# Kernel tuning notes

Measured on AMD Instinct MI355X. Metric: run time of the kernel, lower is better.

Reference implementation:

```python
import jax, jax.numpy as jnp
import numpy as np

C = 512
CQK = C // 8  # 64


def setup_inputs() -> dict:
    key = jax.random.key(0)
    ks = jax.random.split(key, 7)
    s = 0.02
    x = jax.random.normal(ks[0], (4, C, 64, 64), dtype=jnp.float32)
    Wq = jax.random.normal(ks[1], (CQK, C), dtype=jnp.float32) * s
    bq = jnp.zeros((CQK,), dtype=jnp.float32)
    Wk = jax.random.normal(ks[2], (CQK, C), dtype=jnp.float32) * s
    bk = jnp.zeros((CQK,), dtype=jnp.float32)
    Wv = jax.random.normal(ks[3], (C, C), dtype=jnp.float32) * s
    bv = jnp.zeros((C,), dtype=jnp.float32)
    return {"x": x, "Wq": Wq, "bq": bq, "Wk": Wk, "bk": bk, "Wv": Wv, "bv": bv}


def reference(x, Wq, bq, Wk, bk, Wv, bv):
    B, Cc, W, H = x.shape
    N = W * H
    xf = x.reshape(B, Cc, N)  # [B, C, N]
    # 1x1 convs are channel-wise matmuls
    q = jnp.einsum('oc,bcn->bon', Wq, xf) + bq[None, :, None]  # [B, CQK, N]
    k = jnp.einsum('oc,bcn->bon', Wk, xf) + bk[None, :, None]  # [B, CQK, N]
    v = jnp.einsum('oc,bcn->bon', Wv, xf) + bv[None, :, None]  # [B, C, N]
    # attention[b, i, j] = softmax_j(q_i . k_j)
    scores = jnp.einsum('bqi,bqj->bij', q, k)  # [B, N, N]
    attn = jax.nn.softmax(scores, axis=-1)
    # out[b, c, i] = sum_j v[b, c, j] * attn[b, i, j]
    out = jnp.einsum('bcj,bij->bci', v, attn)
    return out.reshape(B, Cc, W, H) + x
```

## Files before the change

kernel.cpp:

```cpp
#include <hip/hip_runtime.h>


typedef __attribute__((ext_vector_type(8))) short bf16x8;
typedef __attribute__((ext_vector_type(4))) float f32x4;

#define MFMA16(A, B, C) __builtin_amdgcn_mfma_f32_16x16x32_bf16((A), (B), (C), 0, 0, 0)
#define MFMA8(A, B, C) __builtin_amdgcn_mfma_f32_16x16x32_fp8_fp8((long)(A), (long)(B), (C), 0, 0, 0)

__device__ __forceinline__ ushort f2bf(float f) {
  uint u = __builtin_bit_cast(uint, f);
  u = (u + 0x7FFFu + ((u >> 16) & 1u)) >> 16;
  return (ushort)u;
}

__device__ __forceinline__ void gload_lds16(const void* g, void* l) {
  __builtin_amdgcn_global_load_lds(
      (const __attribute__((address_space(1))) void*)g,
      (__attribute__((address_space(3))) void*)l, 16, 0, 0);
}

__device__ __forceinline__ void lds_barrier() {
  __builtin_amdgcn_sched_barrier(0);
  asm volatile("s_waitcnt lgkmcnt(0)" ::: "memory");
  __builtin_amdgcn_s_barrier();
  __builtin_amdgcn_sched_barrier(0);
}

__global__ void wconv(const float* __restrict__ Wq, const float* __restrict__ Wk,
                      const float* __restrict__ Wv, ushort* __restrict__ Wb) {
  const int row = blockIdx.x;
  const int t = threadIdx.x;
  const float* src = row < 64 ? Wq + (size_t)row * 512
                   : row < 128 ? Wk + (size_t)(row - 64) * 512
                               : Wv + (size_t)(row - 128) * 512;
  const float4 f = *reinterpret_cast<const float4*>(src + t * 4);
  ushort4 u;
  u.x = f2bf(f.x); u.y = f2bf(f.y); u.z = f2bf(f.z); u.w = f2bf(f.w);
  *reinterpret_cast<ushort4*>(Wb + (size_t)row * 512 + t * 4) = u;
}

__global__ __launch_bounds__(512, 1) void qkv_fused(
    const float* __restrict__ x, const ushort* __restrict__ Wb,
    const float* __restrict__ bq, const float* __restrict__ bk,
    const float* __restrict__ bv,
    ushort* __restrict__ q, ushort* __restrict__ k, uchar* __restrict__ v) {
  __shared__ ushort xT[64][72];

  const int bid = blockIdx.x;
  const int xcd = bid & 7;
  const int b = xcd >> 1;
  const int n0 = ((bid >> 3) + ((xcd & 1) << 5)) * 64;
  const int tid = threadIdx.x;
  const int w = tid >> 6, l = tid & 63;
  const int l15 = l & 15, l16 = l >> 4;

  const float* xb = x + (size_t)b * 512 * 4096 + n0;

  float xr[8];
#define LOADX(CH0)                                              \
  _Pragma("unroll") for (int p = 0; p < 8; ++p)                 \
      xr[p] = xb[((size_t)((CH0) + w * 8 + p)) * 4096 + l];

  LOADX(0);

  const f32x4 fz = {0.f, 0.f, 0.f, 0.f};
  f32x4 acc[4][5];
#pragma unroll
  for (int a = 0; a < 4; ++a)
#pragma unroll
    for (int o = 0; o < 5; ++o) acc[a][o] = fz;

  for (int ck = 0; ck < 8; ++ck) {
    bf16x8 xw;
#pragma unroll
    for (int p = 0; p < 8; ++p) xw[p] = (short)f2bf(xr[p]);
    *reinterpret_cast<bf16x8*>(&xT[l][w * 8]) = xw;
    lds_barrier();
    if (ck < 7) {
      const int c1 = (ck + 1) * 64;
      LOADX(c1);
    }
#pragma unroll
    for (int kk = 0; kk < 2; ++kk) {
      bf16x8 a[4];
#pragma unroll
      for (int nf = 0; nf < 4; ++nf)
        a[nf] = *reinterpret_cast<const bf16x8*>(&xT[nf * 16 + l15][kk * 32 + l16 * 8]);
#pragma unroll
      for (int oi = 0; oi < 5; ++oi) {
        const bf16x8 bw = *reinterpret_cast<const bf16x8*>(
            &Wb[(size_t)(w * 80 + oi * 16 + l15) * 512 + ck * 64 + kk * 32 + l16 * 8]);
#pragma unroll
        for (int nf = 0; nf < 4; ++nf) acc[nf][oi] = MFMA16(a[nf], bw, acc[nf][oi]);
      }
    }
    lds_barrier();
  }

#pragma unroll
  for (int oi = 0; oi < 5; ++oi) {
    const int obase = w * 80 + oi * 16;
    const int orow = obase + l15;
    if (obase < 64) {
      const float bias = bq[orow];
      ushort* dq = q + ((size_t)b * 4096 + n0) * 64;
#pragma unroll
      for (int nf = 0; nf < 4; ++nf)
#pragma unroll
        for (int r = 0; r < 4; ++r)
          dq[(size_t)(nf * 16 + l16 * 4 + r) * 64 + orow] = f2bf(acc[nf][oi][r] + bias);
    } else if (obase < 128) {
      const float bias = bk[orow - 64];
      ushort* dk = k + ((size_t)b * 4096 + n0) * 64;
#pragma unroll
      for (int nf = 0; nf < 4; ++nf)
#pragma unroll
        for (int r = 0; r < 4; ++r)
          dk[(size_t)(nf * 16 + l16 * 4 + r) * 64 + (orow - 64)] = f2bf(acc[nf][oi][r] + bias);
    } else {
      const int c = orow - 128;
      const float bias = bv[c];
#pragma unroll
      for (int nf = 0; nf < 4; ++nf) {
        uint u = 0;
        u = __builtin_amdgcn_cvt_pk_fp8_f32(acc[nf][oi][0] + bias, acc[nf][oi][1] + bias, u, false);
        u = __builtin_amdgcn_cvt_pk_fp8_f32(acc[nf][oi][2] + bias, acc[nf][oi][3] + bias, u, true);
        *reinterpret_cast<uint*>(&v[((size_t)b * 512 + c) * 4096 + n0 + nf * 16 + l16 * 4]) = u;
      }
    }
  }
}

__global__ __launch_bounds__(256, 2) void attn_kernel(
    const float* __restrict__ x, const ushort* __restrict__ q,
    const ushort* __restrict__ k, const uchar* __restrict__ v,
    float* __restrict__ out) {
  __shared__ uchar vbuf[2][32768];
  __shared__ uchar kbuf[2][8192];

  const int bid = blockIdx.x;
  const int xcd = bid & 7;
  const int b = xcd >> 1;
  const int i0 = ((bid >> 3) + ((xcd & 1) << 6)) * 32;
  const int tid = threadIdx.x;
  const int w = tid >> 6, l = tid & 63;
  const int l15 = l & 15, l16 = l >> 4;
  const int hi = l >> 5;
  const int rg = w & 1, ch = w >> 1;
  const int i0w = i0 + rg * 16;
  const int c0 = ch * 256;

  const uchar* kbb = (const uchar*)(k + (size_t)b * 4096 * 64);
  const uchar* vg = v + (size_t)b * 512 * 4096;

  bf16x8 qf0, qf1;
  {
    const ushort* qp = q + ((size_t)b * 4096 + i0w + l15) * 64 + l16 * 8;
    qf0 = *reinterpret_cast<const bf16x8*>(qp);
    qf1 = *reinterpret_cast<const bf16x8*>(qp + 32);
  }

  const int vrow = tid >> 2;
  const int vslot = tid & 3;
  const uchar* vstage = vg + (size_t)vrow * 4096 + (size_t)(((2 * vslot) ^ (vrow & 6)) * 8);
  uchar* vdst = &vbuf[0][0] + vrow * 64 + vslot * 16;

  const int krow = tid >> 3;
  const int kslot = tid & 7;
  const uchar* kstage = kbb + (size_t)krow * 128 + (size_t)(((kslot ^ (krow & 7)) & 7) * 16);
  uchar* kdst = &kbuf[0][0] + tid * 16;

  const int krd0 = (l16 ^ (l15 & 7)) * 16;
  const int krd1 = ((4 ^ l16) ^ (l15 & 7)) * 16;

  const int voff0 = l15 * 64 + ((l16 ^ (l15 & 6)) * 8);
  const int voff1 = l15 * 64 + (((4 ^ l16) ^ (l15 & 6)) * 8);
  const int choff = ch * 16384;

  const int src0 = l15 + ((l16 & 1) << 5);
  const int src1 = src0 + 16;

  const f32x4 fz = {0.f, 0.f, 0.f, 0.f};
  f32x4 acc[16];
#pragma unroll
  for (int ct = 0; ct < 16; ++ct) acc[ct] = fz;
  float l_acc = 0.f;

#define STAGE(J0, NB)                                                         \
  {                                                                           \
    const uchar* _vs = vstage + (J0);                                         \
    uchar* _vd = vdst + (NB) * 32768;                                         \
    _Pragma("unroll") for (int r = 0; r < 8; ++r)                             \
        gload_lds16(_vs + (size_t)r * 64 * 4096, _vd + r * 4096);             \
    const uchar* _ks = kstage + (size_t)(J0) * 128;                           \
    uchar* _kd = kdst + (NB) * 8192;                                          \
    _Pragma("unroll") for (int r = 0; r < 2; ++r)                             \
        gload_lds16(_ks + (size_t)r * 32 * 128, _kd + r * 4096);              \
  }

  STAGE(0, 0);

  for (int t = 0; t < 64; ++t) {
    const int cur = t & 1;
    const int jn = ((t + 1) & 63) * 64;

    __builtin_amdgcn_sched_barrier(0);
    asm volatile("s_barrier" ::: "memory");
    __builtin_amdgcn_sched_barrier(0);

    STAGE(jn, cur ^ 1);

    __builtin_amdgcn_sched_barrier(0);
    asm volatile("s_waitcnt vmcnt(10)" ::: "memory");
    __builtin_amdgcn_sched_barrier(0);
    asm volatile("s_barrier" ::: "memory");
    __builtin_amdgcn_sched_barrier(0);

    const uchar* kB = &kbuf[cur][0];
    uint u[4];
#pragma unroll
    for (int tt = 0; tt < 4; ++tt) {
      const int row = tt * 16 + l15;
      const bf16x8 kc0 = *reinterpret_cast<const bf16x8*>(kB + row * 128 + krd0);
      const bf16x8 kc1 = *reinterpret_cast<const bf16x8*>(kB + row * 128 + krd1);
      f32x4 s = fz;
      s = MFMA16(kc0, qf0, s);
      s = MFMA16(kc1, qf1, s);
      const float p0 = __expf(s[0] - 5.f);
      const float p1 = __expf(s[1] - 5.f);
      const float p2 = __expf(s[2] - 5.f);
      const float p3 = __expf(s[3] - 5.f);
      l_acc += (p0 + p1) + (p2 + p3);
      uint pu = 0;
      pu = __builtin_amdgcn_cvt_pk_fp8_f32(p0, p1, pu, false);
      pu = __builtin_amdgcn_cvt_pk_fp8_f32(p2, p3, pu, true);
      u[tt] = pu;
    }

    const uint a0 = __shfl(u[0], src0), b0 = __shfl(u[1], src0);
    const uint a1 = __shfl(u[0], src1), b1 = __shfl(u[1], src1);
    const uint e0 = __shfl(u[2], src0), f0 = __shfl(u[3], src0);
    const uint e1 = __shfl(u[2], src1), f1 = __shfl(u[3], src1);
    const ulong pa0 = (ulong)(hi ? b0 : a0) | ((ulong)(hi ? b1 : a1) << 32);
    const ulong pa1 = (ulong)(hi ? f0 : e0) | ((ulong)(hi ? f1 : e1) << 32);

    const uchar* vB = &vbuf[cur][0] + choff;
    __builtin_amdgcn_s_setprio(1);
#pragma unroll
    for (int ct = 0; ct < 16; ++ct) {
      const ulong v0 = *reinterpret_cast<const ulong*>(vB + ct * 1024 + voff0);
      const ulong v1 = *reinterpret_cast<const ulong*>(vB + ct * 1024 + voff1);
      acc[ct] = MFMA8(pa0, v0, acc[ct]);
      acc[ct] = MFMA8(pa1, v1, acc[ct]);
    }
    __builtin_amdgcn_s_setprio(0);
  }

  asm volatile("s_waitcnt vmcnt(0)" ::: "memory");
  __builtin_amdgcn_sched_barrier(0);
  asm volatile("s_barrier" ::: "memory");
  __builtin_amdgcn_sched_barrier(0);

  float* l_sm = reinterpret_cast<float*>(&kbuf[0][0]);
  l_acc += __shfl_xor(l_acc, 16);
  l_acc += __shfl_xor(l_acc, 32);
  if (l < 16) l_sm[w * 16 + l] = l_acc;
  __builtin_amdgcn_sched_barrier(0);
  asm volatile("s_waitcnt lgkmcnt(0)" ::: "memory");
  __builtin_amdgcn_sched_barrier(0);

  float linv[4];
#pragma unroll
  for (int r = 0; r < 4; ++r) linv[r] = 1.f / l_sm[w * 16 + l16 * 4 + r];

#pragma unroll
  for (int ct = 0; ct < 16; ++ct) {
    const int c = c0 + ct * 16 + l15;
    const size_t idx = ((size_t)b * 512 + c) * 4096 + i0w + l16 * 4;
    const float4 xr = *reinterpret_cast<const float4*>(&x[idx]);
    float4 o;
    o.x = acc[ct][0] * linv[0] + xr.x;
    o.y = acc[ct][1] * linv[1] + xr.y;
    o.z = acc[ct][2] * linv[2] + xr.z;
    o.w = acc[ct][3] * linv[3] + xr.w;
    *reinterpret_cast<float4*>(&out[idx]) = o;
  }
}

extern "C" void kernel_launch(void* const* d_in, const int* in_sizes, int n_in,
                              void* d_out, int out_size, void* d_ws, size_t ws_size,
                              hipStream_t stream) {
  const float* x  = (const float*)d_in[0];
  const float* Wq = (const float*)d_in[1];
  const float* bq = (const float*)d_in[2];
  const float* Wk = (const float*)d_in[3];
  const float* bk = (const float*)d_in[4];
  const float* Wv = (const float*)d_in[5];
  const float* bv = (const float*)d_in[6];
  float* out = (float*)d_out;

  ushort* qws = (ushort*)d_ws;
  ushort* kws = qws + (size_t)4 * 4096 * 64;
  uchar*  vws = (uchar*)(kws + (size_t)4 * 4096 * 64);
  ushort* wb  = (ushort*)(vws + (size_t)4 * 512 * 4096);

  wconv<<<dim3(640), 128, 0, stream>>>(Wq, Wk, Wv, wb);
  qkv_fused<<<dim3(256), 512, 0, stream>>>(x, wb, bq, bk, bv, qws, kws, vws);
  attn_kernel<<<dim3(512), 256, 0, stream>>>(x, qws, kws, vws, out);
}
```

Measured before the change: 182.7 us.

## Split QK score computation across wave pairs and share P through LDS

Instead of every wave recomputing the QK^T scores and exp for its 16 query rows, the two waves that share a row group alternate by tile parity: one computes P and writes it to a small padded LDS buffer while the other prefetches K into registers straight from global memory. K is no longer staged in LDS, and the softmax denominator is now accumulated by an extra fp8 MFMA against a ones vector, so the quantized P is also what gets summed. This removes duplicated MFMA/exp work and the cross-lane shuffles, at the cost of an LDS round trip for P, uneven per-wave work each iteration, and register-held K fragments.

After: 169.1 us. 1.08x faster.

```diff
diff --git a/kernel.cpp b/kernel.cpp
--- a/kernel.cpp
+++ b/kernel.cpp
@@ -136,7 +136,7 @@
     const ushort* __restrict__ k, const uchar* __restrict__ v,
     float* __restrict__ out) {
   __shared__ uchar vbuf[2][32768];
-  __shared__ uchar kbuf[2][8192];
+  __shared__ uint Pp[2][2][16 * 18];
 
   const int bid = blockIdx.x;
   const int xcd = bid & 7;
@@ -145,12 +145,11 @@
   const int tid = threadIdx.x;
   const int w = tid >> 6, l = tid & 63;
   const int l15 = l & 15, l16 = l >> 4;
-  const int hi = l >> 5;
   const int rg = w & 1, ch = w >> 1;
   const int i0w = i0 + rg * 16;
   const int c0 = ch * 256;
 
-  const uchar* kbb = (const uchar*)(k + (size_t)b * 4096 * 64);
+  const ushort* kb = k + (size_t)b * 4096 * 64;
   const uchar* vg = v + (size_t)b * 512 * 4096;
 
   bf16x8 qf0, qf1;
@@ -165,43 +164,44 @@
   const uchar* vstage = vg + (size_t)vrow * 4096 + (size_t)(((2 * vslot) ^ (vrow & 6)) * 8);
   uchar* vdst = &vbuf[0][0] + vrow * 64 + vslot * 16;
 
-  const int krow = tid >> 3;
-  const int kslot = tid & 7;
-  const uchar* kstage = kbb + (size_t)krow * 128 + (size_t)(((kslot ^ (krow & 7)) & 7) * 16);
-  uchar* kdst = &kbuf[0][0] + tid * 16;
-
-  const int krd0 = (l16 ^ (l15 & 7)) * 16;
-  const int krd1 = ((4 ^ l16) ^ (l15 & 7)) * 16;
-
   const int voff0 = l15 * 64 + ((l16 ^ (l15 & 6)) * 8);
   const int voff1 = l15 * 64 + (((4 ^ l16) ^ (l15 & 6)) * 8);
   const int choff = ch * 16384;
 
-  const int src0 = l15 + ((l16 & 1) << 5);
-  const int src1 = src0 + 16;
+  const ushort* kl = kb + (size_t)l15 * 64 + l16 * 8;
 
   const f32x4 fz = {0.f, 0.f, 0.f, 0.f};
   f32x4 acc[16];
 #pragma unroll
   for (int ct = 0; ct < 16; ++ct) acc[ct] = fz;
-  float l_acc = 0.f;
+  f32x4 lvec = fz;
+  const ulong ONES8 = 0x3838383838383838UL;
+
+  bf16x8 kc[4][2];
 
 #define STAGE(J0, NB)                                                         \
   {                                                                           \
-    const uchar* _vs = vstage + (J0);                                         \
-    uchar* _vd = vdst + (NB) * 32768;                                         \
+    const uchar* _s = vstage + (J0);                                          \
+    uchar* _d = vdst + (NB) * 32768;                                          \
     _Pragma("unroll") for (int r = 0; r < 8; ++r)                             \
-        gload_lds16(_vs + (size_t)r * 64 * 4096, _vd + r * 4096);             \
-    const uchar* _ks = kstage + (size_t)(J0) * 128;                           \
-    uchar* _kd = kdst + (NB) * 8192;                                          \
-    _Pragma("unroll") for (int r = 0; r < 2; ++r)                             \
-        gload_lds16(_ks + (size_t)r * 32 * 128, _kd + r * 4096);              \
-  }
-
+        gload_lds16(_s + (size_t)r * 64 * 4096, _d + r * 4096);               \
+  }
+
+#define KLOAD(J0)                                                             \
+  {                                                                           \
+    _Pragma("unroll") for (int tt = 0; tt < 4; ++tt) {                        \
+      const ushort* kp = kl + (size_t)((J0) + tt * 16) * 64;                  \
+      kc[tt][0] = *reinterpret_cast<const bf16x8*>(kp);                       \
+      kc[tt][1] = *reinterpret_cast<const bf16x8*>(kp + 32);                  \
+    }                                                                         \
+  }
+
+  if (ch == 0) KLOAD(0);
   STAGE(0, 0);
 
   for (int t = 0; t < 64; ++t) {
     const int cur = t & 1;
+    const int par = t & 1;
     const int jn = ((t + 1) & 63) * 64;
 
     __builtin_amdgcn_sched_barrier(0);
@@ -209,40 +209,42 @@
     __builtin_amdgcn_sched_barrier(0);
 
     STAGE(jn, cur ^ 1);
-
-    __builtin_amdgcn_sched_barrier(0);
-    asm volatile("s_waitcnt vmcnt(10)" ::: "memory");
+    if (ch != par) KLOAD(jn);
+
+    if (ch == par) {
+      uint* Pw = &Pp[cur][rg][0];
+#pragma unroll
+      for (int tt = 0; tt < 4; ++tt) {
+        f32x4 s = fz;
+        s = MFMA16(kc[tt][0], qf0, s);
+        s = MFMA16(kc[tt][1], qf1, s);
+        const float p0 = __expf(s[0] - 5.f);
+        const float p1 = __expf(s[1] - 5.f);
+        const float p2 = __expf(s[2] - 5.f);
+        const float p3 = __expf(s[3] - 5.f);
+        uint pu = 0;
+        pu = __builtin_amdgcn_cvt_pk_fp8_f32(p0, p1, pu, false);
+        pu = __builtin_amdgcn_cvt_pk_fp8_f32(p2, p3, pu, true);
+        Pw[l15 * 18 + tt * 4 + l16] = pu;
+      }
+      __builtin_amdgcn_sched_barrier(0);
+      asm volatile("s_waitcnt lgkmcnt(0)" ::: "memory");
+      __builtin_amdgcn_sched_barrier(0);
+      asm volatile("s_waitcnt vmcnt(8)" ::: "memory");
+    } else {
+      asm volatile("s_waitcnt vmcnt(16)" ::: "memory");
+    }
     __builtin_amdgcn_sched_barrier(0);
     asm volatile("s_barrier" ::: "memory");
     __builtin_amdgcn_sched_barrier(0);
 
-    const uchar* kB = &kbuf[cur][0];
-    uint u[4];
-#pragma unroll
-    for (int tt = 0; tt < 4; ++tt) {
-      const int row = tt * 16 + l15;
-      const bf16x8 kc0 = *reinterpret_cast<const bf16x8*>(kB + row * 128 + krd0);
-      const bf16x8 kc1 = *reinterpret_cast<const bf16x8*>(kB + row * 128 + krd1);
-      f32x4 s = fz;
-      s = MFMA16(kc0, qf0, s);
-      s = MFMA16(kc1, qf1, s);
-      const float p0 = __expf(s[0] - 5.f);
-      const float p1 = __expf(s[1] - 5.f);
-      const float p2 = __expf(s[2] - 5.f);
-      const float p3 = __expf(s[3] - 5.f);
-      l_acc += (p0 + p1) + (p2 + p3);
-      uint pu = 0;
-      pu = __builtin_amdgcn_cvt_pk_fp8_f32(p0, p1, pu, false);
-      pu = __builtin_amdgcn_cvt_pk_fp8_f32(p2, p3, pu, true);
-      u[tt] = pu;
-    }
-
-    const uint a0 = __shfl(u[0], src0), b0 = __shfl(u[1], src0);
-    const uint a1 = __shfl(u[0], src1), b1 = __shfl(u[1], src1);
-    const uint e0 = __shfl(u[2], src0), f0 = __shfl(u[3], src0);
-    const uint e1 = __shfl(u[2], src1), f1 = __shfl(u[3], src1);
-    const ulong pa0 = (ulong)(hi ? b0 : a0) | ((ulong)(hi ? b1 : a1) << 32);
-    const ulong pa1 = (ulong)(hi ? f0 : e0) | ((ulong)(hi ? f1 : e1) << 32);
+    const uint* Pr = &Pp[cur][rg][0];
+    const uint lo0 = Pr[l15 * 18 + l16 * 2];
+    const uint hi0 = Pr[l15 * 18 + l16 * 2 + 1];
+    const uint lo1 = Pr[l15 * 18 + 8 + l16 * 2];
+    const uint hi1 = Pr[l15 * 18 + 8 + l16 * 2 + 1];
+    const ulong pa0 = (ulong)lo0 | ((ulong)hi0 << 32);
+    const ulong pa1 = (ulong)lo1 | ((ulong)hi1 << 32);
 
     const uchar* vB = &vbuf[cur][0] + choff;
     __builtin_amdgcn_s_setprio(1);
@@ -253,25 +255,16 @@
       acc[ct] = MFMA8(pa0, v0, acc[ct]);
       acc[ct] = MFMA8(pa1, v1, acc[ct]);
     }
+    lvec = MFMA8(pa0, ONES8, lvec);
+    lvec = MFMA8(pa1, ONES8, lvec);
     __builtin_amdgcn_s_setprio(0);
   }
 
   asm volatile("s_waitcnt vmcnt(0)" ::: "memory");
-  __builtin_amdgcn_sched_barrier(0);
-  asm volatile("s_barrier" ::: "memory");
-  __builtin_amdgcn_sched_barrier(0);
-
-  float* l_sm = reinterpret_cast<float*>(&kbuf[0][0]);
-  l_acc += __shfl_xor(l_acc, 16);
-  l_acc += __shfl_xor(l_acc, 32);
-  if (l < 16) l_sm[w * 16 + l] = l_acc;
-  __builtin_amdgcn_sched_barrier(0);
-  asm volatile("s_waitcnt lgkmcnt(0)" ::: "memory");
-  __builtin_amdgcn_sched_barrier(0);
 
   float linv[4];
 #pragma unroll
-  for (int r = 0; r < 4; ++r) linv[r] = 1.f / l_sm[w * 16 + l16 * 4 + r];
+  for (int r = 0; r < 4; ++r) linv[r] = 1.f / lvec[r];
 
 #pragma unroll
   for (int ct = 0; ct < 16; ++ct) {
```
